# Kernel optimization log

Measured on AMD Instinct MI355X. Metric: run time of the kernel, lower is better.

## Reference

```python
import jax, jax.numpy as jnp
import numpy as np

N_NODES = 100000
N_HID = 128
N_ETYPES = 10
N_EDGES = 100000  # edges per etype


def setup_inputs() -> dict:
    key = jax.random.key(0)
    k1, k2, k3, k4 = jax.random.split(key, 4)
    h = jax.random.normal(k1, (N_NODES, N_HID), dtype=jnp.float32)
    W = jax.random.normal(k2, (N_ETYPES, N_HID), dtype=jnp.float32)
    src = jax.random.randint(k3, (N_ETYPES, N_EDGES), 0, N_NODES, dtype=jnp.int64)
    dst = jax.random.randint(k4, (N_ETYPES, N_EDGES), 0, N_NODES, dtype=jnp.int64)
    rel = jnp.arange(N_ETYPES, dtype=jnp.int64)  # rel2idx: etype -> relation row
    return {"h": h, "W": W, "src": src, "dst": dst, "rel": rel}


def reference(h, W, src, dst, rel):
    # DistMult: score(e) = sum_d h[src_e, d] * W[rel_e, d] * h[dst_e, d]
    h_u = h[src]          # [T, E, d]  gather src features
    h_v = h[dst]          # [T, E, d]  gather dst features
    h_r = W[rel]          # [T, d]     relation embedding per etype
    scores = jnp.einsum('ted,td,ted->te', h_u, h_r, h_v)  # [T, E]
    # pretrain_mode path applies sigmoid per etype
    return jax.nn.sigmoid(scores)
```

## Files before the change

### kernel.cpp

```cpp
#include <hip/hip_runtime.h>
#include <hip/hip_fp16.h>
#include <math.h>

#define N_NODES  100000
#define N_HID    128
#define N_ETYPES 10
#define N_EDGES  100000
#define TOT_EDGES (N_ETYPES * N_EDGES)

#define NSLICE    64
#define SLICE_CAP 16384
#define EPB_SC    2048
#define NBLK_SC   ((TOT_EDGES + EPB_SC - 1) / EPB_SC)
#define NBLK_CV   ((N_NODES * N_HID) / (256 * 8))
#define EPB_SCORE 128
#define NBLK_SCORE (NSLICE * (SLICE_CAP / EPB_SCORE))

#define EDGES_PER_HW 4

typedef __attribute__((ext_vector_type(2))) _Float16 h2v;
typedef __attribute__((ext_vector_type(4))) int i4v;

#if defined(__has_builtin)
#if __has_builtin(__builtin_amdgcn_fdot2)
#define HAVE_FDOT2 1
#endif
#endif

__device__ __forceinline__ float dot2acc(h2v a, h2v b, float c) {
#ifdef HAVE_FDOT2
    return __builtin_amdgcn_fdot2(a, b, c, false);
#else
    return c + (float)a.x * (float)b.x + (float)a.y * (float)b.y;
#endif
}

template<int CTRL>
__device__ __forceinline__ float ror_add(float p) {
    int r = __builtin_amdgcn_update_dpp(0, __float_as_int(p), CTRL, 0xF, 0xF, true);
    return p + __int_as_float(r);
}
__device__ __forceinline__ float row16_sum(float p) {
    p = ror_add<0x121>(p);
    p = ror_add<0x122>(p);
    p = ror_add<0x124>(p);
    p = ror_add<0x128>(p);
    return p;
}

__device__ __forceinline__ float dot_row(uint4 a, uint4 b, uint4 w) {
    union { uint4 u; h2v p[4]; } ua, ub, uw;
    ua.u = a; ub.u = b; uw.u = w;
    float p = dot2acc(ua.p[0], (h2v)(uw.p[0] * ub.p[0]), 0.0f);
    p = dot2acc(ua.p[1], (h2v)(uw.p[1] * ub.p[1]), p);
    p = dot2acc(ua.p[2], (h2v)(uw.p[2] * ub.p[2]), p);
    p = dot2acc(ua.p[3], (h2v)(uw.p[3] * ub.p[3]), p);
    return p;
}


__device__ __forceinline__ void conv_vec8(const float* __restrict__ h,
                                          __half* __restrict__ h16, size_t off) {
    const float4 f0 = *(const float4*)(h + off);
    const float4 f1 = *(const float4*)(h + off + 4);
    union { uint4 u; __half2 p[4]; } pk;
    pk.p[0] = __floats2half2_rn(f0.x, f0.y);
    pk.p[1] = __floats2half2_rn(f0.z, f0.w);
    pk.p[2] = __floats2half2_rn(f1.x, f1.y);
    pk.p[3] = __floats2half2_rn(f1.z, f1.w);
    *(uint4*)(h16 + off) = pk.u;
}

__device__ __forceinline__ void wr16_rows(int tid,
    const float* __restrict__ W, const int* __restrict__ rel,
    __half* __restrict__ Wr16) {
    if (tid < (N_ETYPES * N_HID / 8)) {
        const int j = tid * 8;
        const int t = j >> 7;
        const int c = j & (N_HID - 1);
        const int r = rel[t];
        const float4 g0 = *(const float4*)(W + (size_t)r * N_HID + c);
        const float4 g1 = *(const float4*)(W + (size_t)r * N_HID + c + 4);
        union { uint4 u; __half2 p[4]; } pw;
        pw.p[0] = __floats2half2_rn(g0.x, g0.y);
        pw.p[1] = __floats2half2_rn(g0.z, g0.w);
        pw.p[2] = __floats2half2_rn(g1.x, g1.y);
        pw.p[3] = __floats2half2_rn(g1.z, g1.w);
        *(uint4*)(Wr16 + j) = pw.u;
    }
}

__device__ __forceinline__ void scatter_block(int vb, int tid,
    const int* __restrict__ src, const int* __restrict__ dst,
    int* __restrict__ cursor, uint2* __restrict__ rec,
    int* lcnt, int* lbase) {
    if (tid < NSLICE) lcnt[tid] = 0;
    __syncthreads();

    const int e0 = vb * EPB_SC + tid * 8;
    const bool active = (e0 < TOT_EDGES);

    int ss[8], dd[8], sl[8];
    if (active) {
        const i4v s0 = __builtin_nontemporal_load((const i4v*)(src + e0));
        const i4v s1 = __builtin_nontemporal_load((const i4v*)(src + e0 + 4));
        const i4v d0 = __builtin_nontemporal_load((const i4v*)(dst + e0));
        const i4v d1 = __builtin_nontemporal_load((const i4v*)(dst + e0 + 4));
        ss[0]=s0.x; ss[1]=s0.y; ss[2]=s0.z; ss[3]=s0.w;
        ss[4]=s1.x; ss[5]=s1.y; ss[6]=s1.z; ss[7]=s1.w;
        dd[0]=d0.x; dd[1]=d0.y; dd[2]=d0.z; dd[3]=d0.w;
        dd[4]=d1.x; dd[5]=d1.y; dd[6]=d1.z; dd[7]=d1.w;
        #pragma unroll
        for (int k = 0; k < 8; ++k) {
            sl[k] = (int)(((unsigned long long)(unsigned)dd[k] * 1407374884ULL) >> 41);
            atomicAdd(&lcnt[sl[k]], 1);
        }
    }
    __syncthreads();
    if (tid < NSLICE) {
        const int c = lcnt[tid];
        lbase[tid] = c ? (tid * SLICE_CAP + atomicAdd(&cursor[tid], c)) : 0;
        lcnt[tid] = 0;
    }
    __syncthreads();
    if (active) {
        #pragma unroll
        for (int k = 0; k < 8; ++k) {
            const int e   = e0 + k;
            const int ety = (int)(((unsigned long long)(unsigned)e * 1407374884ULL) >> 47);
            const int off = e - ety * N_EDGES;
            const int r   = atomicAdd(&lcnt[sl[k]], 1);
            const int pos = lbase[sl[k]] + r;
            const unsigned lo = (unsigned)ss[k] | ((unsigned)dd[k] << 17);
            const unsigned hi = ((unsigned)dd[k] >> 15) | ((unsigned)ety << 2) | ((unsigned)off << 6);
            rec[pos] = make_uint2(lo, hi);
        }
    }
}

__global__ __launch_bounds__(256) void prep_kernel(
    const float* __restrict__ h, const float* __restrict__ W,
    const int*   __restrict__ rel,
    const int*   __restrict__ src, const int* __restrict__ dst,
    __half* __restrict__ h16, __half* __restrict__ Wr16,
    int* __restrict__ cursor, uint2* __restrict__ rec)
{
    __shared__ int lcnt[NSLICE];
    __shared__ int lbase[NSLICE];
    const int b   = blockIdx.x;
    const int tid = threadIdx.x;
    if (b < NBLK_SC) {
        scatter_block(b, tid, src, dst, cursor, rec, lcnt, lbase);
    } else {
        const int cb = b - NBLK_SC;
        conv_vec8(h, h16, ((size_t)cb * 256 + tid) * 8);
        if (cb == 0) wr16_rows(tid, W, rel, Wr16);
    }
}

__global__ __launch_bounds__(256) void score_kernel(
    const __half* __restrict__ h16,
    const __half* __restrict__ Wr16,
    const uint2*  __restrict__ rec,
    const int*    __restrict__ cursor,
    float*        __restrict__ out)
{
    const int tid  = threadIdx.x;
    const int lane = tid & 63;
    const int g    = lane >> 4;
    const int gl   = lane & 15;
    const int wid  = tid >> 6;

    const int b     = blockIdx.x;
    const int x     = b & 7;
    const int j     = b >> 3;
    const int s     = x + ((j >> 7) << 3);
    const int chunk = j & 127;
    const int sbase = s << 14;
    const int cnt   = cursor[s];
    const unsigned col = (unsigned)gl << 3;

    int e_lo = (chunk << 7) + (wid << 4);
    #pragma unroll 1
    for (int rnd = 0; rnd < 2; ++rnd, e_lo += 64) {
        if (e_lo >= cnt) break;

        const int i0 = e_lo + g;
        const int i1 = e_lo + 4 + g;
        const int i2 = e_lo + 8 + g;
        const int i3 = e_lo + 12 + g;
        const uint2 r0 = rec[sbase + (i0 < cnt ? i0 : 0)];
        const uint2 r1 = rec[sbase + (i1 < cnt ? i1 : 0)];
        const uint2 r2 = rec[sbase + (i2 < cnt ? i2 : 0)];
        const uint2 r3 = rec[sbase + (i3 < cnt ? i3 : 0)];

        const unsigned s0 = r0.x & 131071u, d0 = ((r0.x >> 17) | (r0.y << 15)) & 131071u;
        const unsigned t0 = (r0.y >> 2) & 15u,  o0 = r0.y >> 6;
        const unsigned s1 = r1.x & 131071u, d1 = ((r1.x >> 17) | (r1.y << 15)) & 131071u;
        const unsigned t1 = (r1.y >> 2) & 15u,  o1 = r1.y >> 6;
        const unsigned s2 = r2.x & 131071u, d2 = ((r2.x >> 17) | (r2.y << 15)) & 131071u;
        const unsigned t2 = (r2.y >> 2) & 15u,  o2 = r2.y >> 6;
        const unsigned s3 = r3.x & 131071u, d3 = ((r3.x >> 17) | (r3.y << 15)) & 131071u;
        const unsigned t3 = (r3.y >> 2) & 15u,  o3 = r3.y >> 6;

        const uint4 Wv0 = *(const uint4*)(Wr16 + ((t0 << 7) + col));
        const uint4 Wv1 = *(const uint4*)(Wr16 + ((t1 << 7) + col));
        const uint4 Wv2 = *(const uint4*)(Wr16 + ((t2 << 7) + col));
        const uint4 Wv3 = *(const uint4*)(Wr16 + ((t3 << 7) + col));
        const uint4 A0 = *(const uint4*)(h16 + ((s0 << 7) + col));
        const uint4 B0 = *(const uint4*)(h16 + ((d0 << 7) + col));
        const uint4 A1 = *(const uint4*)(h16 + ((s1 << 7) + col));
        const uint4 B1 = *(const uint4*)(h16 + ((d1 << 7) + col));
        const uint4 A2 = *(const uint4*)(h16 + ((s2 << 7) + col));
        const uint4 B2 = *(const uint4*)(h16 + ((d2 << 7) + col));
        const uint4 A3 = *(const uint4*)(h16 + ((s3 << 7) + col));
        const uint4 B3 = *(const uint4*)(h16 + ((d3 << 7) + col));

        float p0 = row16_sum(dot_row(A0, B0, Wv0));
        float p1 = row16_sum(dot_row(A1, B1, Wv1));
        float p2 = row16_sum(dot_row(A2, B2, Wv2));
        float p3 = row16_sum(dot_row(A3, B3, Wv3));

        if (gl < 4) {
            const int ii = e_lo + (gl << 2) + g;
            if (ii < cnt) {
                const float    res = (gl == 0) ? p0 : (gl == 1) ? p1 : (gl == 2) ? p2 : p3;
                const unsigned tt  = (gl == 0) ? t0 : (gl == 1) ? t1 : (gl == 2) ? t2 : t3;
                const unsigned oo  = (gl == 0) ? o0 : (gl == 1) ? o1 : (gl == 2) ? o2 : o3;
                __builtin_nontemporal_store(1.0f / (1.0f + __expf(-res)), out + tt * N_EDGES + oo);
            }
        }
    }
}

__global__ __launch_bounds__(256) void distmult_score_f32_kernel(
    const float* __restrict__ h,
    const float* __restrict__ W,
    const int*   __restrict__ src,
    const int*   __restrict__ dst,
    const int*   __restrict__ rel,
    float*       __restrict__ out)
{
    const int t    = blockIdx.y;
    const int lane = threadIdx.x & 31;
    const int hw   = (blockIdx.x << 3) + (threadIdx.x >> 5);
    const int r = rel[t];
    const float4 w4 = ((const float4*)(W + (size_t)r * N_HID))[lane];
    const long base = (long)t * N_EDGES;
    const int  e0   = hw * EDGES_PER_HW;
    float res = 0.0f;
    #pragma unroll
    for (int k = 0; k < EDGES_PER_HW; ++k) {
        const int e = e0 + k;
        const int s = src[base + e];
        const int d = dst[base + e];
        const float4 a = ((const float4*)(h + (size_t)s * N_HID))[lane];
        const float4 b = ((const float4*)(h + (size_t)d * N_HID))[lane];
        float p = a.x * w4.x * b.x + a.y * w4.y * b.y
                + a.z * w4.z * b.z + a.w * w4.w * b.w;
        p += __shfl_xor(p, 16, 64);
        p += __shfl_xor(p, 8, 64);
        p += __shfl_xor(p, 4, 64);
        p += __shfl_xor(p, 2, 64);
        p += __shfl_xor(p, 1, 64);
        if (lane == k) res = p;
    }
    if (lane < EDGES_PER_HW) {
        out[base + e0 + lane] = 1.0f / (1.0f + __expf(-res));
    }
}

extern "C" void kernel_launch(void* const* d_in, const int* in_sizes, int n_in,
                              void* d_out, int out_size, void* d_ws, size_t ws_size,
                              hipStream_t stream) {
    const float* h   = (const float*)d_in[0];
    const float* W   = (const float*)d_in[1];
    const int*   src = (const int*)d_in[2];
    const int*   dst = (const int*)d_in[3];
    const int*   rel = (const int*)d_in[4];
    float*       out = (float*)d_out;

    const size_t h16_bytes  = (size_t)N_NODES * N_HID * sizeof(__half);
    const size_t wr16_bytes = 4096;
    const size_t rec_bytes  = (size_t)NSLICE * SLICE_CAP * 8;
    const size_t cur_bytes  = 4096;
    const size_t need_full  = h16_bytes + wr16_bytes + rec_bytes + cur_bytes;

    if (ws_size >= need_full) {
        char* w = (char*)d_ws;
        __half* h16    = (__half*)w;   w += h16_bytes;
        __half* Wr16   = (__half*)w;   w += wr16_bytes;
        uint2*  rec    = (uint2*)w;    w += rec_bytes;
        int*    cursor = (int*)w;

        (void)hipMemsetAsync(cursor, 0, NSLICE * sizeof(int), stream);
        prep_kernel<<<NBLK_SC + NBLK_CV, 256, 0, stream>>>(
            h, W, rel, src, dst, h16, Wr16, cursor, rec);
        score_kernel<<<NBLK_SCORE, 256, 0, stream>>>(h16, Wr16, rec, cursor, out);
    } else {
        dim3 grid(N_EDGES / (8 * EDGES_PER_HW), N_ETYPES);
        distmult_score_f32_kernel<<<grid, 256, 0, stream>>>(h, W, src, dst, rel, out);
    }
}
```

Measured before the change: 153.1 us.

## Stage per-slice destination node rows in LDS and use finer dst slicing

Edges are now bucketed into 512 destination slices instead of 64. Each score block handles one whole slice: it first copies that slice's contiguous range of fp16 node rows into shared memory, then reads destination features from LDS while source rows and relation rows are still gathered from global memory. This halves the random global gathers per edge. Cursor counters are padded to separate cache lines to cut atomic contention. The costs are a fixed 50KB LDS footprint per block, a smaller grid with lower occupancy, and a fixed slice capacity that could overflow for skewed dst distributions (the count is clamped in the score kernel, but the scatter step does not check it).

```diff
diff --git a/kernel.cpp b/kernel.cpp
--- a/kernel.cpp
+++ b/kernel.cpp
@@ -8,13 +8,13 @@
 #define N_EDGES  100000
 #define TOT_EDGES (N_ETYPES * N_EDGES)
 
-#define NSLICE    64
-#define SLICE_CAP 16384
+#define NSLICE    512
+#define SLICE_CAP 2304
+#define MAXROWS   196
+#define CPAD      16
 #define EPB_SC    2048
 #define NBLK_SC   ((TOT_EDGES + EPB_SC - 1) / EPB_SC)
 #define NBLK_CV   ((N_NODES * N_HID) / (256 * 8))
-#define EPB_SCORE 128
-#define NBLK_SCORE (NSLICE * (SLICE_CAP / EPB_SCORE))
 
 #define EDGES_PER_HW 4
 
@@ -94,7 +94,7 @@
     const int* __restrict__ src, const int* __restrict__ dst,
     int* __restrict__ cursor, uint2* __restrict__ rec,
     int* lcnt, int* lbase) {
-    if (tid < NSLICE) lcnt[tid] = 0;
+    for (int i = tid; i < NSLICE; i += 256) lcnt[i] = 0;
     __syncthreads();
 
     const int e0 = vb * EPB_SC + tid * 8;
@@ -112,15 +112,15 @@
         dd[4]=d1.x; dd[5]=d1.y; dd[6]=d1.z; dd[7]=d1.w;
         #pragma unroll
         for (int k = 0; k < 8; ++k) {
-            sl[k] = (int)(((unsigned long long)(unsigned)dd[k] * 1407374884ULL) >> 41);
+            sl[k] = (int)(((unsigned long long)(unsigned)dd[k] * 1407374884ULL) >> 38);
             atomicAdd(&lcnt[sl[k]], 1);
         }
     }
     __syncthreads();
-    if (tid < NSLICE) {
-        const int c = lcnt[tid];
-        lbase[tid] = c ? (tid * SLICE_CAP + atomicAdd(&cursor[tid], c)) : 0;
-        lcnt[tid] = 0;
+    for (int i = tid; i < NSLICE; i += 256) {
+        const int c = lcnt[i];
+        lbase[i] = c ? (i * SLICE_CAP + atomicAdd(&cursor[i * CPAD], c)) : 0;
+        lcnt[i] = 0;
     }
     __syncthreads();
     if (active) {
@@ -158,71 +158,71 @@
     }
 }
 
-__global__ __launch_bounds__(256) void score_kernel(
+#define DECODE(r, sN, dN, tN, oN) \
+    const unsigned sN = r.x & 131071u; \
+    const unsigned dN = ((r.x >> 17) | (r.y << 15)) & 131071u; \
+    const unsigned tN = (r.y >> 2) & 15u; \
+    const unsigned oN = r.y >> 6;
+
+__global__ __launch_bounds__(512, 4) void score_kernel(
     const __half* __restrict__ h16,
     const __half* __restrict__ Wr16,
     const uint2*  __restrict__ rec,
     const int*    __restrict__ cursor,
     float*        __restrict__ out)
 {
+    __shared__ uint4 lds[MAXROWS * 16];
+
     const int tid  = threadIdx.x;
     const int lane = tid & 63;
     const int g    = lane >> 4;
     const int gl   = lane & 15;
     const int wid  = tid >> 6;
 
-    const int b     = blockIdx.x;
-    const int x     = b & 7;
-    const int j     = b >> 3;
-    const int s     = x + ((j >> 7) << 3);
-    const int chunk = j & 127;
-    const int sbase = s << 14;
-    const int cnt   = cursor[s];
+    const int s     = blockIdx.x;
+    const int nbase = (s * 100000 + 511) >> 9;
+    const int nend  = ((s + 1) * 100000 + 511) >> 9;
+    const int nvec  = (nend - nbase) << 4;
+
+    const uint4* hsrc = (const uint4*)h16 + ((size_t)nbase << 4);
+    for (int i = tid; i < nvec; i += 512) lds[i] = hsrc[i];
+    __syncthreads();
+
+    int cnt = cursor[s * CPAD];
+    if (cnt > SLICE_CAP) cnt = SLICE_CAP;
+    const int sbase = s * SLICE_CAP;
     const unsigned col = (unsigned)gl << 3;
 
-    int e_lo = (chunk << 7) + (wid << 4);
-    #pragma unroll 1
-    for (int rnd = 0; rnd < 2; ++rnd, e_lo += 64) {
-        if (e_lo >= cnt) break;
-
-        const int i0 = e_lo + g;
-        const int i1 = e_lo + 4 + g;
-        const int i2 = e_lo + 8 + g;
-        const int i3 = e_lo + 12 + g;
+    for (int e0 = wid << 4; e0 < cnt; e0 += 512 * 16 / 64) {
+        const int i0 = e0 + g, i1 = e0 + 4 + g, i2 = e0 + 8 + g, i3 = e0 + 12 + g;
         const uint2 r0 = rec[sbase + (i0 < cnt ? i0 : 0)];
         const uint2 r1 = rec[sbase + (i1 < cnt ? i1 : 0)];
         const uint2 r2 = rec[sbase + (i2 < cnt ? i2 : 0)];
         const uint2 r3 = rec[sbase + (i3 < cnt ? i3 : 0)];
 
-        const unsigned s0 = r0.x & 131071u, d0 = ((r0.x >> 17) | (r0.y << 15)) & 131071u;
-        const unsigned t0 = (r0.y >> 2) & 15u,  o0 = r0.y >> 6;
-        const unsigned s1 = r1.x & 131071u, d1 = ((r1.x >> 17) | (r1.y << 15)) & 131071u;
-        const unsigned t1 = (r1.y >> 2) & 15u,  o1 = r1.y >> 6;
-        const unsigned s2 = r2.x & 131071u, d2 = ((r2.x >> 17) | (r2.y << 15)) & 131071u;
-        const unsigned t2 = (r2.y >> 2) & 15u,  o2 = r2.y >> 6;
-        const unsigned s3 = r3.x & 131071u, d3 = ((r3.x >> 17) | (r3.y << 15)) & 131071u;
-        const unsigned t3 = (r3.y >> 2) & 15u,  o3 = r3.y >> 6;
-
-        const uint4 Wv0 = *(const uint4*)(Wr16 + ((t0 << 7) + col));
-        const uint4 Wv1 = *(const uint4*)(Wr16 + ((t1 << 7) + col));
-        const uint4 Wv2 = *(const uint4*)(Wr16 + ((t2 << 7) + col));
-        const uint4 Wv3 = *(const uint4*)(Wr16 + ((t3 << 7) + col));
+        DECODE(r0, s0, d0, t0, o0)  DECODE(r1, s1, d1, t1, o1)
+        DECODE(r2, s2, d2, t2, o2)  DECODE(r3, s3, d3, t3, o3)
+
         const uint4 A0 = *(const uint4*)(h16 + ((s0 << 7) + col));
-        const uint4 B0 = *(const uint4*)(h16 + ((d0 << 7) + col));
         const uint4 A1 = *(const uint4*)(h16 + ((s1 << 7) + col));
-        const uint4 B1 = *(const uint4*)(h16 + ((d1 << 7) + col));
         const uint4 A2 = *(const uint4*)(h16 + ((s2 << 7) + col));
-        const uint4 B2 = *(const uint4*)(h16 + ((d2 << 7) + col));
         const uint4 A3 = *(const uint4*)(h16 + ((s3 << 7) + col));
-        const uint4 B3 = *(const uint4*)(h16 + ((d3 << 7) + col));
-
-        float p0 = row16_sum(dot_row(A0, B0, Wv0));
-        float p1 = row16_sum(dot_row(A1, B1, Wv1));
-        float p2 = row16_sum(dot_row(A2, B2, Wv2));
-        float p3 = row16_sum(dot_row(A3, B3, Wv3));
+        const uint4 W0 = *(const uint4*)(Wr16 + ((t0 << 7) + col));
+        const uint4 W1 = *(const uint4*)(Wr16 + ((t1 << 7) + col));
+        const uint4 W2 = *(const uint4*)(Wr16 + ((t2 << 7) + col));
+        const uint4 W3 = *(const uint4*)(Wr16 + ((t3 << 7) + col));
+        const uint4 B0 = lds[(((int)d0 - nbase) << 4) + gl];
+        const uint4 B1 = lds[(((int)d1 - nbase) << 4) + gl];
+        const uint4 B2 = lds[(((int)d2 - nbase) << 4) + gl];
+        const uint4 B3 = lds[(((int)d3 - nbase) << 4) + gl];
+
+        const float p0 = row16_sum(dot_row(A0, B0, W0));
+        const float p1 = row16_sum(dot_row(A1, B1, W1));
+        const float p2 = row16_sum(dot_row(A2, B2, W2));
+        const float p3 = row16_sum(dot_row(A3, B3, W3));
 
         if (gl < 4) {
-            const int ii = e_lo + (gl << 2) + g;
+            const int ii = e0 + (gl << 2) + g;
             if (ii < cnt) {
                 const float    res = (gl == 0) ? p0 : (gl == 1) ? p1 : (gl == 2) ? p2 : p3;
                 const unsigned tt  = (gl == 0) ? t0 : (gl == 1) ? t1 : (gl == 2) ? t2 : t3;
@@ -283,7 +283,7 @@
     const size_t h16_bytes  = (size_t)N_NODES * N_HID * sizeof(__half);
     const size_t wr16_bytes = 4096;
     const size_t rec_bytes  = (size_t)NSLICE * SLICE_CAP * 8;
-    const size_t cur_bytes  = 4096;
+    const size_t cur_bytes  = (size_t)NSLICE * CPAD * sizeof(int);
     const size_t need_full  = h16_bytes + wr16_bytes + rec_bytes + cur_bytes;
 
     if (ws_size >= need_full) {
@@ -293,10 +293,10 @@
         uint2*  rec    = (uint2*)w;    w += rec_bytes;
         int*    cursor = (int*)w;
 
-        (void)hipMemsetAsync(cursor, 0, NSLICE * sizeof(int), stream);
+        (void)hipMemsetAsync(cursor, 0, cur_bytes, stream);
         prep_kernel<<<NBLK_SC + NBLK_CV, 256, 0, stream>>>(
             h, W, rel, src, dst, h16, Wr16, cursor, rec);
-        score_kernel<<<NBLK_SCORE, 256, 0, stream>>>(h16, Wr16, rec, cursor, out);
+        score_kernel<<<NSLICE, 512, 0, stream>>>(h16, Wr16, rec, cursor, out);
     } else {
         dim3 grid(N_EDGES / (8 * EDGES_PER_HW), N_ETYPES);
         distmult_score_f32_kernel<<<grid, 256, 0, stream>>>(h, W, src, dst, rel, out);
```

New measurement: 166.4 us. 1.09x slower.
